# Optimization experiments

Measured on AMD Instinct MI355X. Metric: run time of the kernel, lower is better.

Reference implementation:

```python
import math
import jax, jax.numpy as jnp
import numpy as np

N_HEADS = 8

def setup_inputs() -> dict:
    key = jax.random.key(0)
    k1, k2 = jax.random.split(key)
    b, c, n = 8, 512, 2048  # c = n_heads * d = 8 * 64
    qkv = jax.random.normal(k1, (b, 3 * c, n), dtype=jnp.float32)
    mask = jax.random.uniform(k2, (b, n)) > 0.1
    return {"qkv": qkv, "mask": mask}

def reference(qkv, mask):
    b, width, n = qkv.shape
    m = N_HEADS
    assert width % (3 * m) == 0
    d = width // (3 * m)
    # 'b (m D) n -> (b m) D n' with D = 3d, then split into q, k, v
    x = qkv.reshape(b, m, 3 * d, n).reshape(b * m, 3 * d, n)
    q, k, v = x[:, :d], x[:, d:2 * d], x[:, 2 * d:]
    scale = 1.0 / math.sqrt(math.sqrt(d))
    # (B, i, j) attention logits, B = b*m
    weight = jnp.einsum('Bdi,Bdj->Bij', q * scale, k * scale)
    # mask: 'b j -> (b m) () j'
    mkey = jnp.broadcast_to(mask[:, None, None, :], (b, m, 1, n)).reshape(b * m, 1, n)
    neg = -jnp.finfo(weight.dtype).max
    weight = jnp.where(mkey, weight, neg)
    weight = jax.nn.softmax(weight, axis=-1)
    a = jnp.einsum('Bin,Bdn->Bdi', weight, v)  # (b*m, d, n)
    return a.reshape(b, m, d, n).reshape(b, m * d, n)
```

## Files before the change

kernel.cpp:

```cpp
#include <hip/hip_runtime.h>
#include <hip/hip_bf16.h>


typedef __attribute__((ext_vector_type(8))) short short8;
typedef __attribute__((ext_vector_type(4))) float f32x4;
typedef __attribute__((ext_vector_type(4))) unsigned int u32x4;

#define SEQ 2048
#define DH 64
#define NH 8
#define NHEADS_TOT 64
#define NTILES 32
#define TILE_BYTES 8192
#define IMG_MAT (NHEADS_TOT * NTILES * TILE_BYTES)
#define WS_NEED (3 * (size_t)IMG_MAT + 65536)
#define LOG2E 1.4426950408889634f

__device__ __forceinline__ unsigned short f2b(float f) {
  unsigned int u = __float_as_uint(f);
  u += 0x7FFFu + ((u >> 16) & 1u);
  return (unsigned short)(u >> 16);
}
__device__ __forceinline__ unsigned int pk2(float a, float b) {
  return (unsigned int)f2b(a) | ((unsigned int)f2b(b) << 16);
}
__device__ __forceinline__ unsigned int cvtpk(float lo, float hi) {
  unsigned int r;
  asm("v_cvt_pk_bf16_f32 %0, %1, %2" : "=v"(r) : "v"(lo), "v"(hi));
  return r;
}
union pkcast { u32x4 u; short8 s; };

__global__ __launch_bounds__(256)
void qkv_prep(const float* __restrict__ qkv, const void* __restrict__ mraw,
              char* __restrict__ ws) {
  __shared__ float Lf[64 * 68];
  __shared__ int flag;
  const int tid = threadIdx.x;
  const int b = blockIdx.x;

  if (b >= 3 * NHEADS_TOT * NTILES) {
    const int bi = b - 3 * NHEADS_TOT * NTILES;
    if (tid == 0) flag = 0;
    __syncthreads();
    const int* mi = (const int*)mraw;
    int bad = 0;
    for (int idx = tid; idx < 4096; idx += 256) {
      int v = mi[idx];
      bad |= (v != 0) & (v != 1);
    }
    if (bad) atomicOr(&flag, 1);
    __syncthreads();
    const bool isByte = (flag != 0);
    float* mb = (float*)(ws + 3 * (size_t)IMG_MAT) + bi * SEQ;
    for (int j = tid; j < SEQ; j += 256) {
      bool keep = isByte ? (((const unsigned char*)mraw)[bi * SEQ + j] != 0)
                         : (((const int*)mraw)[bi * SEQ + j] != 0);
      mb[j] = keep ? (-8.0f * LOG2E) : (-60008.0f * LOG2E);
    }
    return;
  }

  const int m = b / (NHEADS_TOT * NTILES);
  const int rem = b - m * (NHEADS_TOT * NTILES);
  const int head = rem >> 5;
  const int t = rem & 31;
  const int bi = head >> 3, h = head & 7;
  const float* src = qkv + (size_t)bi * (3 * NH * DH * SEQ)
                         + (size_t)h * (3 * DH * SEQ)
                         + (size_t)m * (DH * SEQ);
  char* img = ws + (size_t)m * IMG_MAT + (size_t)(head * NTILES + t) * TILE_BYTES;

  const int trow = tid >> 4;
  const int tj4 = (tid & 15) * 4;
  #pragma unroll
  for (int p = 0; p < 4; ++p) {
    int dd = p * 16 + trow;
    float4 v = *(const float4*)(src + (size_t)dd * SEQ + t * 64 + tj4);
    *(float4*)(&Lf[dd * 68 + tj4]) = v;
  }
  __syncthreads();

  #pragma unroll
  for (int qq = 0; qq < 2; ++qq) {
    int q = tid * 2 + qq;
    int row = q >> 3;
    int cp = q & 7;
    int c = cp ^ (row & 7);
    unsigned int u[4];
    if (m == 2) {
      #pragma unroll
      for (int e2 = 0; e2 < 4; ++e2) {
        float a = Lf[row * 68 + c * 8 + e2 * 2];
        float bb = Lf[row * 68 + c * 8 + e2 * 2 + 1];
        u[e2] = pk2(a, bb);
      }
    } else {
      #pragma unroll
      for (int e2 = 0; e2 < 4; ++e2) {
        float a = Lf[(c * 8 + e2 * 2) * 68 + row];
        float bb = Lf[(c * 8 + e2 * 2 + 1) * 68 + row];
        u[e2] = pk2(a, bb);
      }
    }
    u32x4 uv = { u[0], u[1], u[2], u[3] };
    *(u32x4*)(img + q * 16) = uv;
  }
}

#define KOFF 0
#define VOFF 16384
#define MBOFF 32768
#define SMEMB 33280

__device__ __forceinline__ void async16(const void* g, void* l) {
  __builtin_amdgcn_global_load_lds(
      (const __attribute__((address_space(1))) void*)g,
      (__attribute__((address_space(3))) void*)l, 16, 0, 0);
}

__global__ __launch_bounds__(256, 4)
void qkv_attn2(const char* __restrict__ ws, float* __restrict__ out) {
  __shared__ __align__(16) char smem[SMEMB];
  const int tid = threadIdx.x;
  const int w = tid >> 6;
  const int lane = tid & 63;
  const int l15 = lane & 15;
  const int g = lane >> 4;
  const int l7 = l15 & 7;

  const int L = blockIdx.x;
  const int head = (L & 7) * 8 + ((L >> 3) >> 4);
  const int qblk = (L >> 3) & 15;
  const int bi = head >> 3, h = head & 7;

  const char* Qimg = ws + (size_t)(head * NTILES + qblk * 2) * TILE_BYTES;
  const char* Kimg = ws + (size_t)IMG_MAT + (size_t)(head * NTILES) * TILE_BYTES;
  const char* Vimg = ws + 2 * (size_t)IMG_MAT + (size_t)(head * NTILES) * TILE_BYTES;
  const float* mbias = (const float*)(ws + 3 * (size_t)IMG_MAT) + bi * SEQ;

  short8 qb[2][2];
  {
    const char* qt = Qimg + (w >> 1) * TILE_BYTES;
    const int rbase = (w & 1) * 32;
    #pragma unroll
    for (int mt = 0; mt < 2; ++mt)
      #pragma unroll
      for (int kk = 0; kk < 2; ++kk) {
        int row = rbase + mt * 16 + l15;
        int cp = (kk * 4 + g) ^ l7;
        qb[mt][kk] = *(const short8*)(qt + row * 128 + cp * 16);
      }
  }

  int kOff[4][2];
  #pragma unroll
  for (int f = 0; f < 4; ++f) {
    int row = 8 * (l15 >> 2) + (l15 & 3) + 4 * (f & 1) + 32 * (f >> 1);
    int r7 = row & 7;
    kOff[f][0] = row * 128 + (((0 + g) ^ r7) * 16);
    kOff[f][1] = row * 128 + (((4 + g) ^ r7) * 16);
  }
  int vOff[4][2];
  #pragma unroll
  for (int nt = 0; nt < 4; ++nt) {
    int vrow = nt * 16 + l15;
    vOff[nt][0] = vrow * 128 + (((0 + g) ^ l7) * 16);
    vOff[nt][1] = vrow * 128 + (((4 + g) ^ l7) * 16);
  }

  const int stOff = (w * 2 * 64 + lane) * 16;

  auto stage = [&](int buf, int tt) {
    const char* kt = Kimg + (size_t)tt * TILE_BYTES + stOff;
    const char* vt = Vimg + (size_t)tt * TILE_BYTES + stOff;
    char* kl = smem + KOFF + buf * 8192 + (w * 2) * 1024;
    char* vl = smem + VOFF + buf * 8192 + (w * 2) * 1024;
    async16(kt, kl);
    async16(kt + 1024, kl + 1024);
    async16(vt, vl);
    async16(vt + 1024, vl + 1024);
    if (tid < 16) {
      f32x4 mv = *(const f32x4*)(mbias + tt * 64 + tid * 4);
      *(f32x4*)(smem + MBOFF + buf * 256 + tid * 16) = mv;
    }
  };

  stage(0, 0);
  __syncthreads();

  f32x4 accO[2][4];
  #pragma unroll
  for (int mt = 0; mt < 2; ++mt)
    #pragma unroll
    for (int nt = 0; nt < 4; ++nt)
      accO[mt][nt] = (f32x4){0.f, 0.f, 0.f, 0.f};
  float lsum[2] = {0.f, 0.f};

  for (int t = 0; t < NTILES; ++t) {
    const int cur = t & 1;
    if (t + 1 < NTILES) stage(cur ^ 1, t + 1);

    const char* Kl = smem + KOFF + cur * 8192;
    f32x4 sAcc[2][4];
    __builtin_amdgcn_s_setprio(1);
    #pragma unroll
    for (int f = 0; f < 4; ++f) {
      short8 kb0 = *(const short8*)(Kl + kOff[f][0]);
      short8 kb1 = *(const short8*)(Kl + kOff[f][1]);
      #pragma unroll
      for (int mt = 0; mt < 2; ++mt) {
        f32x4 z = (f32x4){0.f, 0.f, 0.f, 0.f};
        z = __builtin_amdgcn_mfma_f32_16x16x32_bf16(kb0, qb[mt][0], z, 0, 0, 0);
        z = __builtin_amdgcn_mfma_f32_16x16x32_bf16(kb1, qb[mt][1], z, 0, 0, 0);
        sAcc[mt][f] = z;
      }
    }
    __builtin_amdgcn_s_setprio(0);

    const float* mbL = (const float*)(smem + MBOFF + cur * 256);
    f32x4 mb4[4];
    #pragma unroll
    for (int f = 0; f < 4; ++f)
      mb4[f] = *(const f32x4*)(mbL + 32 * (f >> 1) + 8 * g + 4 * (f & 1));

    short8 pa[2][2];
    #pragma unroll
    for (int mt = 0; mt < 2; ++mt) {
      float pv[4][4];
      float rs = 0.f;
      #pragma unroll
      for (int f = 0; f < 4; ++f)
        #pragma unroll
        for (int r = 0; r < 4; ++r) {
          float p = __builtin_exp2f(
              fmaf(sAcc[mt][f][r], 0.125f * LOG2E, mb4[f][r]));
          pv[f][r] = p;
          rs += p;
        }
      pkcast lo, hi;
      lo.u = (u32x4){ cvtpk(pv[0][0], pv[0][1]), cvtpk(pv[0][2], pv[0][3]),
                      cvtpk(pv[1][0], pv[1][1]), cvtpk(pv[1][2], pv[1][3]) };
      hi.u = (u32x4){ cvtpk(pv[2][0], pv[2][1]), cvtpk(pv[2][2], pv[2][3]),
                      cvtpk(pv[3][0], pv[3][1]), cvtpk(pv[3][2], pv[3][3]) };
      pa[mt][0] = lo.s;
      pa[mt][1] = hi.s;
      rs += __shfl_xor(rs, 16);
      rs += __shfl_xor(rs, 32);
      lsum[mt] += rs;
    }

    const char* Vl = smem + VOFF + cur * 8192;
    __builtin_amdgcn_s_setprio(1);
    #pragma unroll
    for (int nt = 0; nt < 4; ++nt) {
      short8 va0 = *(const short8*)(Vl + vOff[nt][0]);
      short8 va1 = *(const short8*)(Vl + vOff[nt][1]);
      #pragma unroll
      for (int mt = 0; mt < 2; ++mt) {
        accO[mt][nt] = __builtin_amdgcn_mfma_f32_16x16x32_bf16(va0, pa[mt][0], accO[mt][nt], 0, 0, 0);
        accO[mt][nt] = __builtin_amdgcn_mfma_f32_16x16x32_bf16(va1, pa[mt][1], accO[mt][nt], 0, 0, 0);
      }
    }
    __builtin_amdgcn_s_setprio(0);
    __syncthreads();
  }

  float* obase = out + (size_t)bi * (NH * DH * SEQ) + (size_t)h * (DH * SEQ);
  const int i0 = qblk * 128 + w * 32;
  #pragma unroll
  for (int mt = 0; mt < 2; ++mt) {
    float rl = 1.0f / lsum[mt];
    int icol = i0 + mt * 16 + l15;
    #pragma unroll
    for (int nt = 0; nt < 4; ++nt)
      #pragma unroll
      for (int r = 0; r < 4; ++r) {
        int dd = nt * 16 + g * 4 + r;
        obase[(size_t)dd * SEQ + icol] = accO[mt][nt][r] * rl;
      }
  }
}

#define QT0 64
#define KT0 64
#define LDK0 72
#define OFF_QT0 0
#define OFF_KT0 9216
#define OFF_VL0 18432
#define OFF_P0  27648
#define OFF_MB0 36864
#define OFF_L0  37120
#define OFF_FLAG0 37376
#define SMEM_BYTES0 37408
#define NEG_BIG 3.0e38f

__device__ __forceinline__ float b2f(unsigned short s) {
  return __uint_as_float(((unsigned int)s) << 16);
}

__global__ __launch_bounds__(256, 2)
void qkv_attn_fused(const float* __restrict__ qkv,
                    const void* __restrict__ mraw,
                    float* __restrict__ out) {
  __shared__ __align__(16) char smem[SMEM_BYTES0];
  unsigned short* Qt = (unsigned short*)(smem + OFF_QT0);
  unsigned short* Kt = (unsigned short*)(smem + OFF_KT0);
  unsigned short* Vl = (unsigned short*)(smem + OFF_VL0);
  unsigned short* P  = (unsigned short*)(smem + OFF_P0);
  float* mb_lds = (float*)(smem + OFF_MB0);
  float* l_lds  = (float*)(smem + OFF_L0);
  int* flag = (int*)(smem + OFF_FLAG0);

  const int tid  = threadIdx.x;
  const int w    = tid >> 6;
  const int lane = tid & 63;
  const int l15  = lane & 15;
  const int g    = lane >> 4;
  const int dbase = g * 8;

  if (tid == 0) *flag = 0;
  __syncthreads();
  {
    const int* mi = (const int*)mraw;
    int bad = 0;
    for (int idx = tid; idx < 4096; idx += 256) {
      int v = mi[idx];
      bad |= (v != 0) & (v != 1);
    }
    if (bad) atomicOr(flag, 1);
  }
  __syncthreads();
  const bool maskIsByte = (*flag != 0);

  const int L = blockIdx.x;
  const int head  = (L & 7) * 8 + (L >> 8);
  const int qtile = (L >> 3) & 31;
  const int bi = head >> 3;
  const int h  = head & 7;
  const int i0 = qtile * QT0;

  const float* qbase = qkv + (size_t)bi * (3 * NH * DH * SEQ)
                           + (size_t)h * (3 * DH * SEQ);
  const float* kbase = qbase + DH * SEQ;
  const float* vbase = qbase + 2 * DH * SEQ;
  const unsigned char* mb8 = (const unsigned char*)mraw + (size_t)bi * SEQ;
  const int* mb32 = (const int*)mraw + (size_t)bi * SEQ;

  const int trow = tid >> 4;
  const int tj4  = (tid & 15) * 4;

  #pragma unroll
  for (int p = 0; p < 4; ++p) {
    int dd = p * 16 + trow;
    float4 v4 = *(const float4*)(qbase + (size_t)dd * SEQ + i0 + tj4);
    Qt[(tj4 + 0) * LDK0 + dd] = f2b(v4.x);
    Qt[(tj4 + 1) * LDK0 + dd] = f2b(v4.y);
    Qt[(tj4 + 2) * LDK0 + dd] = f2b(v4.z);
    Qt[(tj4 + 3) * LDK0 + dd] = f2b(v4.w);
  }
  __syncthreads();

  const short8 qa0 = *(const short8*)(&Qt[(w * 16 + l15) * LDK0 + dbase]);
  const short8 qa1 = *(const short8*)(&Qt[(w * 16 + l15) * LDK0 + 32 + dbase]);

  f32x4 accO[4];
  #pragma unroll
  for (int nt = 0; nt < 4; ++nt) accO[nt] = (f32x4){0.f, 0.f, 0.f, 0.f};
  float M[4], l[4];
  #pragma unroll
  for (int r = 0; r < 4; ++r) { M[r] = -NEG_BIG; l[r] = 0.0f; }

  for (int t = 0; t < (SEQ / KT0); ++t) {
    const int j0 = t * KT0;
    __syncthreads();

    #pragma unroll
    for (int p = 0; p < 4; ++p) {
      int dd = p * 16 + trow;
      float4 k4 = *(const float4*)(kbase + (size_t)dd * SEQ + j0 + tj4);
      Kt[(tj4 + 0) * LDK0 + dd] = f2b(k4.x);
      Kt[(tj4 + 1) * LDK0 + dd] = f2b(k4.y);
      Kt[(tj4 + 2) * LDK0 + dd] = f2b(k4.z);
      Kt[(tj4 + 3) * LDK0 + dd] = f2b(k4.w);
      float4 vv4 = *(const float4*)(vbase + (size_t)dd * SEQ + j0 + tj4);
      unsigned int lo = (unsigned int)f2b(vv4.x) | ((unsigned int)f2b(vv4.y) << 16);
      unsigned int hi = (unsigned int)f2b(vv4.z) | ((unsigned int)f2b(vv4.w) << 16);
      *(uint2*)(&Vl[dd * LDK0 + tj4]) = make_uint2(lo, hi);
    }
    if (tid < KT0) {
      int j = j0 + tid;
      bool keep = maskIsByte ? (mb8[j] != 0) : (mb32[j] != 0);
      mb_lds[tid] = keep ? 0.0f : -60000.0f;
    }
    __syncthreads();

    f32x4 sAcc[4];
    #pragma unroll
    for (int f = 0; f < 4; ++f) {
      f32x4 z = (f32x4){0.f, 0.f, 0.f, 0.f};
      short8 kb0 = *(const short8*)(&Kt[(f * 16 + l15) * LDK0 + dbase]);
      short8 kb1 = *(const short8*)(&Kt[(f * 16 + l15) * LDK0 + 32 + dbase]);
      z = __builtin_amdgcn_mfma_f32_16x16x32_bf16(qa0, kb0, z, 0, 0, 0);
      z = __builtin_amdgcn_mfma_f32_16x16x32_bf16(qa1, kb1, z, 0, 0, 0);
      sAcc[f] = z;
    }

    float mbf[4];
    #pragma unroll
    for (int f = 0; f < 4; ++f) mbf[f] = mb_lds[f * 16 + l15];

    float s[4][4];
    float rmax[4];
    #pragma unroll
    for (int r = 0; r < 4; ++r) rmax[r] = -NEG_BIG;
    #pragma unroll
    for (int f = 0; f < 4; ++f) {
      #pragma unroll
      for (int r = 0; r < 4; ++r) {
        s[f][r] = sAcc[f][r] * 0.125f + mbf[f];
        rmax[r] = fmaxf(rmax[r], s[f][r]);
      }
    }
    #pragma unroll
    for (int r = 0; r < 4; ++r) {
      rmax[r] = fmaxf(rmax[r], __shfl_xor(rmax[r], 1));
      rmax[r] = fmaxf(rmax[r], __shfl_xor(rmax[r], 2));
      rmax[r] = fmaxf(rmax[r], __shfl_xor(rmax[r], 4));
      rmax[r] = fmaxf(rmax[r], __shfl_xor(rmax[r], 8));
    }
    float alpha[4], newM[4];
    #pragma unroll
    for (int r = 0; r < 4; ++r) {
      newM[r] = fmaxf(M[r], rmax[r]);
      alpha[r] = __expf(M[r] - newM[r]);
      M[r] = newM[r];
    }
    unsigned short pb[4][4];
    float rsum[4] = {0.f, 0.f, 0.f, 0.f};
    #pragma unroll
    for (int f = 0; f < 4; ++f) {
      #pragma unroll
      for (int r = 0; r < 4; ++r) {
        float pvv = __expf(s[f][r] - newM[r]);
        unsigned short bb = f2b(pvv);
        pb[f][r] = bb;
        rsum[r] += b2f(bb);
      }
    }
    #pragma unroll
    for (int r = 0; r < 4; ++r) {
      rsum[r] += __shfl_xor(rsum[r], 1);
      rsum[r] += __shfl_xor(rsum[r], 2);
      rsum[r] += __shfl_xor(rsum[r], 4);
      rsum[r] += __shfl_xor(rsum[r], 8);
      l[r] = l[r] * alpha[r] + rsum[r];
    }
    #pragma unroll
    for (int nt = 0; nt < 4; ++nt) {
      #pragma unroll
      for (int r = 0; r < 4; ++r) accO[nt][r] *= alpha[r];
    }

    unsigned short* Pw = P + w * 16 * LDK0;
    #pragma unroll
    for (int f = 0; f < 4; ++f) {
      #pragma unroll
      for (int r = 0; r < 4; ++r)
        Pw[(g * 4 + r) * LDK0 + f * 16 + l15] = pb[f][r];
    }
    short8 pa0 = *(const short8*)(&Pw[l15 * LDK0 + dbase]);
    short8 pa1 = *(const short8*)(&Pw[l15 * LDK0 + 32 + dbase]);

    #pragma unroll
    for (int nt = 0; nt < 4; ++nt) {
      short8 vb0 = *(const short8*)(&Vl[(nt * 16 + l15) * LDK0 + dbase]);
      short8 vb1 = *(const short8*)(&Vl[(nt * 16 + l15) * LDK0 + 32 + dbase]);
      accO[nt] = __builtin_amdgcn_mfma_f32_16x16x32_bf16(pa0, vb0, accO[nt], 0, 0, 0);
      accO[nt] = __builtin_amdgcn_mfma_f32_16x16x32_bf16(pa1, vb1, accO[nt], 0, 0, 0);
    }
  }

  __syncthreads();
  float* O_lds = (float*)smem;
  #pragma unroll
  for (int nt = 0; nt < 4; ++nt) {
    #pragma unroll
    for (int r = 0; r < 4; ++r)
      O_lds[(w * 16 + g * 4 + r) * 68 + nt * 16 + l15] = accO[nt][r];
  }
  if (l15 == 0) {
    #pragma unroll
    for (int r = 0; r < 4; ++r) l_lds[w * 16 + g * 4 + r] = l[r];
  }
  __syncthreads();

  const int ti = tid & 63;
  const int td = tid >> 6;
  const float rl = 1.0f / l_lds[ti];
  float* obase = out + (size_t)bi * (NH * DH * SEQ)
                     + (size_t)h * (DH * SEQ) + i0 + ti;
  #pragma unroll
  for (int p = 0; p < 16; ++p) {
    int dd = p * 4 + td;
    obase[(size_t)dd * SEQ] = O_lds[ti * 68 + dd] * rl;
  }
}

extern "C" void kernel_launch(void* const* d_in, const int* in_sizes, int n_in,
                              void* d_out, int out_size, void* d_ws, size_t ws_size,
                              hipStream_t stream) {
  const float* qkv = (const float*)d_in[0];
  const void* mask = d_in[1];
  float* out = (float*)d_out;
  (void)in_sizes; (void)n_in; (void)out_size;

  if (ws_size >= WS_NEED && d_ws != nullptr) {
    char* ws = (char*)d_ws;
    qkv_prep<<<dim3(3 * NHEADS_TOT * NTILES + 8), dim3(256), 0, stream>>>(qkv, mask, ws);
    qkv_attn2<<<dim3(1024), dim3(256), 0, stream>>>(ws, out);
  } else {
    qkv_attn_fused<<<dim3(2048), dim3(256), 0, stream>>>(qkv, mask, out);
  }
}
```

Baseline: 140.9 us.

## Fold key mask into V and compute softmax denominator via MFMA

The key-padding mask is no longer added as a per-column bias before exp. Masked columns of V are zeroed during prep, and the row sum is computed by an extra MFMA against a bf16 0/1 mask vector. This removes the per-tile mask bias loads and the cross-lane shuffle reductions for the row sum. The cost is two extra MFMAs per tile, with the row sum now accumulated from bf16-rounded probabilities. Masked columns still produce unmasked exp values in P, which is mathematically equivalent only because their V and denominator contributions are zeroed.

```diff
diff --git a/kernel.cpp b/kernel.cpp
--- a/kernel.cpp
+++ b/kernel.cpp
@@ -35,6 +35,7 @@
 void qkv_prep(const float* __restrict__ qkv, const void* __restrict__ mraw,
               char* __restrict__ ws) {
   __shared__ float Lf[64 * 68];
+  __shared__ float mcol[64];
   __shared__ int flag;
   const int tid = threadIdx.x;
   const int b = blockIdx.x;
@@ -52,11 +53,11 @@
     if (bad) atomicOr(&flag, 1);
     __syncthreads();
     const bool isByte = (flag != 0);
-    float* mb = (float*)(ws + 3 * (size_t)IMG_MAT) + bi * SEQ;
+    unsigned short* mo = (unsigned short*)(ws + 3 * (size_t)IMG_MAT) + bi * SEQ;
     for (int j = tid; j < SEQ; j += 256) {
       bool keep = isByte ? (((const unsigned char*)mraw)[bi * SEQ + j] != 0)
                          : (((const int*)mraw)[bi * SEQ + j] != 0);
-      mb[j] = keep ? (-8.0f * LOG2E) : (-60008.0f * LOG2E);
+      mo[j] = keep ? 0x3F80 : 0;
     }
     return;
   }
@@ -71,6 +72,26 @@
                          + (size_t)m * (DH * SEQ);
   char* img = ws + (size_t)m * IMG_MAT + (size_t)(head * NTILES + t) * TILE_BYTES;
 
+  if (m == 2) {
+    if (tid == 0) flag = 0;
+    __syncthreads();
+    const int* mi = (const int*)mraw;
+    int bad = 0;
+    for (int idx = tid; idx < 4096; idx += 256) {
+      int v = mi[idx];
+      bad |= (v != 0) & (v != 1);
+    }
+    if (bad) atomicOr(&flag, 1);
+    __syncthreads();
+    const bool isByte = (flag != 0);
+    if (tid < 64) {
+      int j = t * 64 + tid;
+      bool keep = isByte ? (((const unsigned char*)mraw)[bi * SEQ + j] != 0)
+                         : (((const int*)mraw)[bi * SEQ + j] != 0);
+      mcol[tid] = keep ? 1.0f : 0.0f;
+    }
+  }
+
   const int trow = tid >> 4;
   const int tj4 = (tid & 15) * 4;
   #pragma unroll
@@ -91,8 +112,9 @@
     if (m == 2) {
       #pragma unroll
       for (int e2 = 0; e2 < 4; ++e2) {
-        float a = Lf[row * 68 + c * 8 + e2 * 2];
-        float bb = Lf[row * 68 + c * 8 + e2 * 2 + 1];
+        int cc = c * 8 + e2 * 2;
+        float a = Lf[row * 68 + cc] * mcol[cc];
+        float bb = Lf[row * 68 + cc + 1] * mcol[cc + 1];
         u[e2] = pk2(a, bb);
       }
     } else {
@@ -110,8 +132,8 @@
 
 #define KOFF 0
 #define VOFF 16384
-#define MBOFF 32768
-#define SMEMB 33280
+#define MOFF 32768
+#define SMEMB 36864
 
 __device__ __forceinline__ void async16(const void* g, void* l) {
   __builtin_amdgcn_global_load_lds(
@@ -137,7 +159,7 @@
   const char* Qimg = ws + (size_t)(head * NTILES + qblk * 2) * TILE_BYTES;
   const char* Kimg = ws + (size_t)IMG_MAT + (size_t)(head * NTILES) * TILE_BYTES;
   const char* Vimg = ws + 2 * (size_t)IMG_MAT + (size_t)(head * NTILES) * TILE_BYTES;
-  const float* mbias = (const float*)(ws + 3 * (size_t)IMG_MAT) + bi * SEQ;
+  const char* m01g = ws + 3 * (size_t)IMG_MAT + (size_t)bi * (SEQ * 2);
 
   short8 qb[2][2];
   {
@@ -180,12 +202,9 @@
     async16(kt + 1024, kl + 1024);
     async16(vt, vl);
     async16(vt + 1024, vl + 1024);
-    if (tid < 16) {
-      f32x4 mv = *(const f32x4*)(mbias + tt * 64 + tid * 4);
-      *(f32x4*)(smem + MBOFF + buf * 256 + tid * 16) = mv;
-    }
   };
 
+  async16(m01g + w * 1024 + lane * 16, smem + MOFF + w * 1024);
   stage(0, 0);
   __syncthreads();
 
@@ -195,7 +214,12 @@
     #pragma unroll
     for (int nt = 0; nt < 4; ++nt)
       accO[mt][nt] = (f32x4){0.f, 0.f, 0.f, 0.f};
-  float lsum[2] = {0.f, 0.f};
+  f32x4 accL[2];
+  accL[0] = (f32x4){0.f, 0.f, 0.f, 0.f};
+  accL[1] = (f32x4){0.f, 0.f, 0.f, 0.f};
+
+  constexpr float SC = 0.125f * LOG2E;
+  constexpr float C8 = -8.0f * LOG2E;
 
   for (int t = 0; t < NTILES; ++t) {
     const int cur = t & 1;
@@ -218,26 +242,15 @@
     }
     __builtin_amdgcn_s_setprio(0);
 
-    const float* mbL = (const float*)(smem + MBOFF + cur * 256);
-    f32x4 mb4[4];
-    #pragma unroll
-    for (int f = 0; f < 4; ++f)
-      mb4[f] = *(const f32x4*)(mbL + 32 * (f >> 1) + 8 * g + 4 * (f & 1));
-
     short8 pa[2][2];
     #pragma unroll
     for (int mt = 0; mt < 2; ++mt) {
       float pv[4][4];
-      float rs = 0.f;
       #pragma unroll
       for (int f = 0; f < 4; ++f)
         #pragma unroll
-        for (int r = 0; r < 4; ++r) {
-          float p = __builtin_exp2f(
-              fmaf(sAcc[mt][f][r], 0.125f * LOG2E, mb4[f][r]));
-          pv[f][r] = p;
-          rs += p;
-        }
+        for (int r = 0; r < 4; ++r)
+          pv[f][r] = __builtin_exp2f(fmaf(sAcc[mt][f][r], SC, C8));
       pkcast lo, hi;
       lo.u = (u32x4){ cvtpk(pv[0][0], pv[0][1]), cvtpk(pv[0][2], pv[0][3]),
                       cvtpk(pv[1][0], pv[1][1]), cvtpk(pv[1][2], pv[1][3]) };
@@ -245,9 +258,15 @@
                       cvtpk(pv[3][0], pv[3][1]), cvtpk(pv[3][2], pv[3][3]) };
       pa[mt][0] = lo.s;
       pa[mt][1] = hi.s;
-      rs += __shfl_xor(rs, 16);
-      rs += __shfl_xor(rs, 32);
-      lsum[mt] += rs;
+    }
+
+    const char* Ml = smem + MOFF + t * 128;
+    short8 mf0 = *(const short8*)(Ml + g * 16);
+    short8 mf1 = *(const short8*)(Ml + 64 + g * 16);
+    #pragma unroll
+    for (int mt = 0; mt < 2; ++mt) {
+      accL[mt] = __builtin_amdgcn_mfma_f32_16x16x32_bf16(mf0, pa[mt][0], accL[mt], 0, 0, 0);
+      accL[mt] = __builtin_amdgcn_mfma_f32_16x16x32_bf16(mf1, pa[mt][1], accL[mt], 0, 0, 0);
     }
 
     const char* Vl = smem + VOFF + cur * 8192;
@@ -270,7 +289,7 @@
   const int i0 = qblk * 128 + w * 32;
   #pragma unroll
   for (int mt = 0; mt < 2; ++mt) {
-    float rl = 1.0f / lsum[mt];
+    float rl = 1.0f / accL[mt][0];
     int icol = i0 + mt * 16 + l15;
     #pragma unroll
     for (int nt = 0; nt < 4; ++nt)
```

New measurement: 124.7 us. -11.5%, faster.
